# Performance work log

Hardware: AMD Instinct MI355X
Metric: run time of the kernel (lower is better)

Reference implementation:

```python
import jax, jax.numpy as jnp
import numpy as np

BLOCK_SIZE = 256
N_EMBED = 384
HEAD_SIZE = 64


def setup_inputs() -> dict:
    key = jax.random.key(0)
    kx, kq, kk, kv = jax.random.split(key, 4)
    B, T = 256, 256
    x = jax.random.normal(kx, (B, T, N_EMBED), dtype=jnp.float32)
    # nn.Linear(n_embed, head_size, bias=False): y = x @ W.T with W [head, embed].
    # We store the transposed weight [embed, head] so forward is x @ W.
    scale = 1.0 / np.sqrt(N_EMBED)
    Wq = jax.random.normal(kq, (N_EMBED, HEAD_SIZE), dtype=jnp.float32) * scale
    Wk = jax.random.normal(kk, (N_EMBED, HEAD_SIZE), dtype=jnp.float32) * scale
    Wv = jax.random.normal(kv, (N_EMBED, HEAD_SIZE), dtype=jnp.float32) * scale
    return {"x": x, "Wq": Wq, "Wk": Wk, "Wv": Wv}


def reference(x, Wq, Wk, Wv):
    B, T, C = x.shape  # C == N_EMBED
    q = jnp.einsum('btc,ch->bth', x, Wq)
    k = jnp.einsum('btc,ch->bth', x, Wk)
    v = jnp.einsum('btc,ch->bth', x, Wv)
    # NOTE: original scales by 1/sqrt(C) where C = embed dim (384), not head_size.
    wei = jnp.einsum('bth,bsh->bts', q, k) / jnp.sqrt(jnp.float32(C))
    causal = jnp.tril(jnp.ones((T, T), dtype=bool))
    wei = jnp.where(causal, wei, -jnp.inf)
    wei = jax.nn.softmax(wei, axis=-1)
    # dropout is identity in eval mode (reference is deterministic)
    out = jnp.einsum('bts,bsh->bth', wei, v)
    return out
```

## Files before the change

### kernel.cpp

```cpp
#include <hip/hip_runtime.h>


typedef short s16x8 __attribute__((ext_vector_type(8)));
typedef float f32x4 __attribute__((ext_vector_type(4)));
typedef float f32x2 __attribute__((ext_vector_type(2)));
typedef unsigned u32x4 __attribute__((ext_vector_type(4)));
typedef __bf16 bf16x2t __attribute__((ext_vector_type(2)));

#define MFMA16(a, b, c) __builtin_amdgcn_mfma_f32_16x16x32_bf16((a), (b), (c), 0, 0, 0)

__device__ __forceinline__ unsigned short f2bf(float f) {
  return __builtin_bit_cast(unsigned short, (__bf16)f);
}
__device__ __forceinline__ unsigned cvt2(float a, float b) {
  f32x2 t; t[0] = a; t[1] = b;
  bf16x2t r = __builtin_convertvector(t, bf16x2t);
  return __builtin_bit_cast(unsigned, r);
}
__device__ __forceinline__ s16x8 cvt8(float4 a, float4 b) {
  u32x4 u;
  u[0] = cvt2(a.x, a.y); u[1] = cvt2(a.z, a.w);
  u[2] = cvt2(b.x, b.y); u[3] = cvt2(b.z, b.w);
  return __builtin_bit_cast(s16x8, u);
}

__global__ __launch_bounds__(256) void wcvt(
    const float* __restrict__ Wq, const float* __restrict__ Wk,
    const float* __restrict__ Wv, unsigned short* __restrict__ Wt_sw) {
  int idx = blockIdx.x * 256 + threadIdx.x;
  int j = idx & 7;
  int c = idx >> 3;
  int n15 = c & 15;
  int q4 = (c >> 4) & 3;
  int g = c >> 6;
  int nt = g % 12;
  int kc = g / 12;
  int n = nt * 16 + n15;
  int kk = kc * 32 + q4 * 8 + j;
  const float* src = (n < 64) ? Wq : (n < 128) ? Wk : Wv;
  float v = src[kk * 64 + (n & 63)];
  if (n < 64) v *= 0.05103103630798287f;
  Wt_sw[idx] = f2bf(v);
}

__global__ __launch_bounds__(512) void fused_attn(
    const float* __restrict__ x, const unsigned short* __restrict__ Wt_sw,
    float* __restrict__ out) {
  __shared__ __align__(16) unsigned short q_l[16384];
  __shared__ __align__(16) unsigned short k_l[16384];
  __shared__ __align__(16) unsigned short v_l[16384];
  __shared__ __align__(16) unsigned short w_l[6144];
  const int b = blockIdx.x;
  const int tid = threadIdx.x;
  const int wv = tid >> 6;
  const int lane = tid & 63;
  const int n15 = lane & 15;
  const int q4 = lane >> 4;

  {
    const int rb0 = wv * 32;
    f32x4 acc[12][2];
#pragma unroll
    for (int i = 0; i < 12; ++i)
#pragma unroll
      for (int t = 0; t < 2; ++t) acc[i][t] = (f32x4){0.f, 0.f, 0.f, 0.f};

    const float* xp0 = x + ((long)b * 256 + rb0 + n15) * 384 + q4 * 8;
    const float* xp1 = xp0 + 16 * 384;
    float4 c00 = *reinterpret_cast<const float4*>(xp0);
    float4 c01 = *reinterpret_cast<const float4*>(xp0 + 4);
    float4 c10 = *reinterpret_cast<const float4*>(xp1);
    float4 c11 = *reinterpret_cast<const float4*>(xp1 + 4);

    const uint4* Wv4 = reinterpret_cast<const uint4*>(Wt_sw);
    uint4* wl4 = reinterpret_cast<uint4*>(w_l);
    uint4 wpa = Wv4[tid];
    uint4 wpb;
    if (tid < 256) wpb = Wv4[512 + tid];

    for (int kc = 0; kc < 12; ++kc) {
      __syncthreads();
      wl4[tid] = wpa;
      if (tid < 256) wl4[512 + tid] = wpb;
      __syncthreads();

      const int nkc = (kc < 11) ? kc + 1 : 11;
      wpa = Wv4[nkc * 768 + tid];
      if (tid < 256) wpb = Wv4[nkc * 768 + 512 + tid];
      float4 p00 = *reinterpret_cast<const float4*>(xp0 + nkc * 32);
      float4 p01 = *reinterpret_cast<const float4*>(xp0 + nkc * 32 + 4);
      float4 p10 = *reinterpret_cast<const float4*>(xp1 + nkc * 32);
      float4 p11 = *reinterpret_cast<const float4*>(xp1 + nkc * 32 + 4);

      s16x8 xa[2];
      xa[0] = cvt8(c00, c01);
      xa[1] = cvt8(c10, c11);

#pragma unroll
      for (int nt = 0; nt < 12; ++nt) {
        s16x8 wf = *reinterpret_cast<const s16x8*>(&w_l[nt * 512 + lane * 8]);
        if (nt < 8) {
          acc[nt][0] = MFMA16(wf, xa[0], acc[nt][0]);
          acc[nt][1] = MFMA16(wf, xa[1], acc[nt][1]);
        } else {
          acc[nt][0] = MFMA16(xa[0], wf, acc[nt][0]);
          acc[nt][1] = MFMA16(xa[1], wf, acc[nt][1]);
        }
      }
      c00 = p00; c01 = p01; c10 = p10; c11 = p11;
    }

#pragma unroll
    for (int t = 0; t < 2; ++t) {
      const int rb = rb0 + t * 16;
      const int qtile = rb >> 4;
#pragma unroll
      for (int mt = 0; mt < 4; ++mt) {
        const int off = ((qtile * 2 + (mt >> 1)) * 64 + (2 * (mt & 1) + (q4 >> 1)) * 16 + n15) * 8
                        + (q4 & 1) * 4;
        uint2 sq, sk;
        sq.x = cvt2(acc[mt][t][0], acc[mt][t][1]);
        sq.y = cvt2(acc[mt][t][2], acc[mt][t][3]);
        sk.x = cvt2(acc[4 + mt][t][0], acc[4 + mt][t][1]);
        sk.y = cvt2(acc[4 + mt][t][2], acc[4 + mt][t][3]);
        *reinterpret_cast<uint2*>(&q_l[off]) = sq;
        *reinterpret_cast<uint2*>(&k_l[off]) = sk;
      }
      const int s0 = rb + q4 * 4;
#pragma unroll
      for (int nt = 0; nt < 4; ++nt) {
        const int off = (((s0 >> 5) * 4 + nt) * 64 + ((s0 >> 3) & 3) * 16 + n15) * 8 + (s0 & 7);
        uint2 sv;
        sv.x = cvt2(acc[8 + nt][t][0], acc[8 + nt][t][1]);
        sv.y = cvt2(acc[8 + nt][t][2], acc[8 + nt][t][3]);
        *reinterpret_cast<uint2*>(&v_l[off]) = sv;
      }
    }
  }
  __syncthreads();

  const int laneA = ((q4 & 1) << 5) + n15;
  const bool hi = (q4 >> 1) != 0;
#pragma unroll
  for (int half = 0; half < 2; ++half) {
    const int qt = half ? (15 - wv) : wv;

    const s16x8 qf0 = *reinterpret_cast<const s16x8*>(&q_l[(qt * 2 + 0) * 512 + lane * 8]);
    const s16x8 qf1 = *reinterpret_cast<const s16x8*>(&q_l[(qt * 2 + 1) * 512 + lane * 8]);

    uint2 pk[16];
    float psum = 0.f;
    s16x8 kf0 = *reinterpret_cast<const s16x8*>(&k_l[0 * 512 + lane * 8]);
    s16x8 kf1 = *reinterpret_cast<const s16x8*>(&k_l[1 * 512 + lane * 8]);
#pragma unroll 16
    for (int ct = 0; ct < 16; ++ct) {
      if (ct > qt) break;
      const int nc = (ct < qt) ? ct + 1 : ct;
      s16x8 nf0 = *reinterpret_cast<const s16x8*>(&k_l[(nc * 2 + 0) * 512 + lane * 8]);
      s16x8 nf1 = *reinterpret_cast<const s16x8*>(&k_l[(nc * 2 + 1) * 512 + lane * 8]);
      f32x4 a = (f32x4){0.f, 0.f, 0.f, 0.f};
      a = MFMA16(kf0, qf0, a);
      a = MFMA16(kf1, qf1, a);
      const bool diag = (ct == qt);
      float p[4];
#pragma unroll
      for (int e = 0; e < 4; ++e) {
        p[e] = (diag && (q4 * 4 + e > n15)) ? 0.f : __expf(a[e]);
        psum += p[e];
      }
      pk[ct].x = cvt2(p[0], p[1]);
      pk[ct].y = cvt2(p[2], p[3]);
      kf0 = nf0; kf1 = nf1;
    }
    psum += __shfl_xor(psum, 16);
    psum += __shfl_xor(psum, 32);
    const float rn_col = 1.0f / psum;

    f32x4 O[4];
#pragma unroll
    for (int nt = 0; nt < 4; ++nt) O[nt] = (f32x4){0.f, 0.f, 0.f, 0.f};
    const int nk = (qt + 2) >> 1;
    s16x8 vf[4], vn[4];
#pragma unroll
    for (int nt = 0; nt < 4; ++nt)
      vf[nt] = *reinterpret_cast<const s16x8*>(&v_l[nt * 512 + lane * 8]);
#pragma unroll 8
    for (int kc = 0; kc < 8; ++kc) {
      if (kc >= nk) break;
      const int ncc = (kc + 1 < nk) ? kc + 1 : kc;
#pragma unroll
      for (int nt = 0; nt < 4; ++nt)
        vn[nt] = *reinterpret_cast<const s16x8*>(&v_l[(ncc * 4 + nt) * 512 + lane * 8]);
      const uint2 t0 = pk[2 * kc];
      const uint2 t1 = (2 * kc + 1 <= qt) ? pk[2 * kc + 1] : make_uint2(0u, 0u);
      unsigned r0a = __shfl(t0.x, laneA),      r0b = __shfl(t0.y, laneA);
      unsigned r0c = __shfl(t0.x, laneA + 16), r0d = __shfl(t0.y, laneA + 16);
      unsigned r1a = __shfl(t1.x, laneA),      r1b = __shfl(t1.y, laneA);
      unsigned r1c = __shfl(t1.x, laneA + 16), r1d = __shfl(t1.y, laneA + 16);
      u32x4 u;
      u[0] = hi ? r1a : r0a; u[1] = hi ? r1b : r0b;
      u[2] = hi ? r1c : r0c; u[3] = hi ? r1d : r0d;
      s16x8 pf = __builtin_bit_cast(s16x8, u);
#pragma unroll
      for (int nt = 0; nt < 4; ++nt) {
        O[nt] = MFMA16(pf, vf[nt], O[nt]);
        vf[nt] = vn[nt];
      }
    }
    float rnm[4];
#pragma unroll
    for (int e = 0; e < 4; ++e) rnm[e] = __shfl(rn_col, q4 * 4 + e);
#pragma unroll
    for (int nt = 0; nt < 4; ++nt)
#pragma unroll
      for (int e = 0; e < 4; ++e)
        out[(size_t)(b * 256 + qt * 16 + q4 * 4 + e) * 64 + nt * 16 + n15] = O[nt][e] * rnm[e];
  }
}

extern "C" void kernel_launch(void* const* d_in, const int* in_sizes, int n_in,
                              void* d_out, int out_size, void* d_ws, size_t ws_size,
                              hipStream_t stream) {
  const float* x  = (const float*)d_in[0];
  const float* Wq = (const float*)d_in[1];
  const float* Wk = (const float*)d_in[2];
  const float* Wv = (const float*)d_in[3];
  float* out = (float*)d_out;

  unsigned short* Wt_sw = (unsigned short*)d_ws;

  wcvt<<<288, 256, 0, stream>>>(Wq, Wk, Wv, Wt_sw);
  fused_attn<<<256, 512, 0, stream>>>(x, Wt_sw, out);
}
```

Before: 173.6 us.

## Use 1024-thread blocks with one query tile per wave and register-resident Q

The block grows from 8 to 16 waves, so each wave projects 16 rows instead of 32 and handles a single causal query tile instead of two balanced halves. Q fragments stay in registers through shuffles, which removes the q_l shared buffer. The weight tile is double-buffered in LDS, cutting one barrier per k-step. The QK^T/exp and PV phases are fused into one loop, so the 16-entry P register array goes away. The trade-off is that per-wave causal work becomes unbalanced (wave 15 does 16 tiles, wave 0 does 1), and the larger block may force fewer registers per thread.

New measurement: 167.4 us. -3.6%, faster.

```diff
diff --git a/kernel.cpp b/kernel.cpp
--- a/kernel.cpp
+++ b/kernel.cpp
@@ -21,6 +21,16 @@
   u32x4 u;
   u[0] = cvt2(a.x, a.y); u[1] = cvt2(a.z, a.w);
   u[2] = cvt2(b.x, b.y); u[3] = cvt2(b.z, b.w);
+  return __builtin_bit_cast(s16x8, u);
+}
+__device__ __forceinline__ s16x8 asm_frag(uint2 t0, uint2 t1, int laneA, bool hi) {
+  unsigned r0a = __shfl(t0.x, laneA),      r0b = __shfl(t0.y, laneA);
+  unsigned r0c = __shfl(t0.x, laneA + 16), r0d = __shfl(t0.y, laneA + 16);
+  unsigned r1a = __shfl(t1.x, laneA),      r1b = __shfl(t1.y, laneA);
+  unsigned r1c = __shfl(t1.x, laneA + 16), r1d = __shfl(t1.y, laneA + 16);
+  u32x4 u;
+  u[0] = hi ? r1a : r0a; u[1] = hi ? r1b : r0b;
+  u[2] = hi ? r1c : r0c; u[3] = hi ? r1d : r0d;
   return __builtin_bit_cast(s16x8, u);
 }
 
@@ -43,13 +53,12 @@
   Wt_sw[idx] = f2bf(v);
 }
 
-__global__ __launch_bounds__(512) void fused_attn(
+__global__ __launch_bounds__(1024, 4) void fused_attn(
     const float* __restrict__ x, const unsigned short* __restrict__ Wt_sw,
     float* __restrict__ out) {
-  __shared__ __align__(16) unsigned short q_l[16384];
   __shared__ __align__(16) unsigned short k_l[16384];
   __shared__ __align__(16) unsigned short v_l[16384];
-  __shared__ __align__(16) unsigned short w_l[6144];
+  __shared__ __align__(16) unsigned short w_l[12288];
   const int b = blockIdx.x;
   const int tid = threadIdx.x;
   const int wv = tid >> 6;
@@ -57,165 +66,135 @@
   const int n15 = lane & 15;
   const int q4 = lane >> 4;
 
-  {
-    const int rb0 = wv * 32;
-    f32x4 acc[12][2];
-#pragma unroll
-    for (int i = 0; i < 12; ++i)
-#pragma unroll
-      for (int t = 0; t < 2; ++t) acc[i][t] = (f32x4){0.f, 0.f, 0.f, 0.f};
-
-    const float* xp0 = x + ((long)b * 256 + rb0 + n15) * 384 + q4 * 8;
-    const float* xp1 = xp0 + 16 * 384;
-    float4 c00 = *reinterpret_cast<const float4*>(xp0);
-    float4 c01 = *reinterpret_cast<const float4*>(xp0 + 4);
-    float4 c10 = *reinterpret_cast<const float4*>(xp1);
-    float4 c11 = *reinterpret_cast<const float4*>(xp1 + 4);
-
-    const uint4* Wv4 = reinterpret_cast<const uint4*>(Wt_sw);
-    uint4* wl4 = reinterpret_cast<uint4*>(w_l);
-    uint4 wpa = Wv4[tid];
-    uint4 wpb;
-    if (tid < 256) wpb = Wv4[512 + tid];
-
-    for (int kc = 0; kc < 12; ++kc) {
-      __syncthreads();
-      wl4[tid] = wpa;
-      if (tid < 256) wl4[512 + tid] = wpb;
-      __syncthreads();
-
-      const int nkc = (kc < 11) ? kc + 1 : 11;
-      wpa = Wv4[nkc * 768 + tid];
-      if (tid < 256) wpb = Wv4[nkc * 768 + 512 + tid];
-      float4 p00 = *reinterpret_cast<const float4*>(xp0 + nkc * 32);
-      float4 p01 = *reinterpret_cast<const float4*>(xp0 + nkc * 32 + 4);
-      float4 p10 = *reinterpret_cast<const float4*>(xp1 + nkc * 32);
-      float4 p11 = *reinterpret_cast<const float4*>(xp1 + nkc * 32 + 4);
-
-      s16x8 xa[2];
-      xa[0] = cvt8(c00, c01);
-      xa[1] = cvt8(c10, c11);
-
-#pragma unroll
-      for (int nt = 0; nt < 12; ++nt) {
-        s16x8 wf = *reinterpret_cast<const s16x8*>(&w_l[nt * 512 + lane * 8]);
-        if (nt < 8) {
-          acc[nt][0] = MFMA16(wf, xa[0], acc[nt][0]);
-          acc[nt][1] = MFMA16(wf, xa[1], acc[nt][1]);
-        } else {
-          acc[nt][0] = MFMA16(xa[0], wf, acc[nt][0]);
-          acc[nt][1] = MFMA16(xa[1], wf, acc[nt][1]);
-        }
-      }
-      c00 = p00; c01 = p01; c10 = p10; c11 = p11;
-    }
-
-#pragma unroll
-    for (int t = 0; t < 2; ++t) {
-      const int rb = rb0 + t * 16;
-      const int qtile = rb >> 4;
-#pragma unroll
-      for (int mt = 0; mt < 4; ++mt) {
-        const int off = ((qtile * 2 + (mt >> 1)) * 64 + (2 * (mt & 1) + (q4 >> 1)) * 16 + n15) * 8
-                        + (q4 & 1) * 4;
-        uint2 sq, sk;
-        sq.x = cvt2(acc[mt][t][0], acc[mt][t][1]);
-        sq.y = cvt2(acc[mt][t][2], acc[mt][t][3]);
-        sk.x = cvt2(acc[4 + mt][t][0], acc[4 + mt][t][1]);
-        sk.y = cvt2(acc[4 + mt][t][2], acc[4 + mt][t][3]);
-        *reinterpret_cast<uint2*>(&q_l[off]) = sq;
-        *reinterpret_cast<uint2*>(&k_l[off]) = sk;
-      }
-      const int s0 = rb + q4 * 4;
-#pragma unroll
-      for (int nt = 0; nt < 4; ++nt) {
-        const int off = (((s0 >> 5) * 4 + nt) * 64 + ((s0 >> 3) & 3) * 16 + n15) * 8 + (s0 & 7);
-        uint2 sv;
-        sv.x = cvt2(acc[8 + nt][t][0], acc[8 + nt][t][1]);
-        sv.y = cvt2(acc[8 + nt][t][2], acc[8 + nt][t][3]);
-        *reinterpret_cast<uint2*>(&v_l[off]) = sv;
-      }
-    }
-  }
-  __syncthreads();
+  f32x4 acc[12];
+#pragma unroll
+  for (int i = 0; i < 12; ++i) acc[i] = (f32x4){0.f, 0.f, 0.f, 0.f};
+
+  const float* xp = x + ((long)b * 256 + wv * 16 + n15) * 384 + q4 * 8;
+  float4 f0a = *reinterpret_cast<const float4*>(xp);
+  float4 f0b = *reinterpret_cast<const float4*>(xp + 4);
+  float4 f1a = *reinterpret_cast<const float4*>(xp + 32);
+  float4 f1b = *reinterpret_cast<const float4*>(xp + 36);
+
+  const uint4* Wv4 = reinterpret_cast<const uint4*>(Wt_sw);
+  uint4* wl4 = reinterpret_cast<uint4*>(w_l);
+  uint4 wreg;
+  if (tid < 768) wreg = Wv4[tid];
+
+  for (int kc = 0; kc < 12; ++kc) {
+    if (tid < 768) wl4[(kc & 1) * 768 + tid] = wreg;
+    __syncthreads();
+    if (kc < 11 && tid < 768) wreg = Wv4[(kc + 1) * 768 + tid];
+    const int nkc = (kc < 10) ? kc + 2 : 11;
+    float4 pa = *reinterpret_cast<const float4*>(xp + nkc * 32);
+    float4 pb = *reinterpret_cast<const float4*>(xp + nkc * 32 + 4);
+
+    s16x8 xa = cvt8(f0a, f0b);
+    const unsigned short* wbuf = w_l + (kc & 1) * 6144;
+#pragma unroll
+    for (int nt = 0; nt < 12; ++nt) {
+      s16x8 wf = *reinterpret_cast<const s16x8*>(&wbuf[nt * 512 + lane * 8]);
+      if (nt < 8) acc[nt] = MFMA16(wf, xa, acc[nt]);
+      else        acc[nt] = MFMA16(xa, wf, acc[nt]);
+    }
+    f0a = f1a; f0b = f1b; f1a = pa; f1b = pb;
+  }
+
+  uint2 pkq[4];
+#pragma unroll
+  for (int mt = 0; mt < 4; ++mt) {
+    pkq[mt].x = cvt2(acc[mt][0], acc[mt][1]);
+    pkq[mt].y = cvt2(acc[mt][2], acc[mt][3]);
+  }
+#pragma unroll
+  for (int mt = 0; mt < 4; ++mt) {
+    const int off = ((wv * 2 + (mt >> 1)) * 64 + (2 * (mt & 1) + (q4 >> 1)) * 16 + n15) * 8
+                    + (q4 & 1) * 4;
+    uint2 sk;
+    sk.x = cvt2(acc[4 + mt][0], acc[4 + mt][1]);
+    sk.y = cvt2(acc[4 + mt][2], acc[4 + mt][3]);
+    *reinterpret_cast<uint2*>(&k_l[off]) = sk;
+  }
+  const int s0 = wv * 16 + q4 * 4;
+#pragma unroll
+  for (int nt = 0; nt < 4; ++nt) {
+    const int off = (((s0 >> 5) * 4 + nt) * 64 + ((s0 >> 3) & 3) * 16 + n15) * 8 + (s0 & 7);
+    uint2 sv;
+    sv.x = cvt2(acc[8 + nt][0], acc[8 + nt][1]);
+    sv.y = cvt2(acc[8 + nt][2], acc[8 + nt][3]);
+    *reinterpret_cast<uint2*>(&v_l[off]) = sv;
+  }
 
   const int laneA = ((q4 & 1) << 5) + n15;
   const bool hi = (q4 >> 1) != 0;
-#pragma unroll
-  for (int half = 0; half < 2; ++half) {
-    const int qt = half ? (15 - wv) : wv;
-
-    const s16x8 qf0 = *reinterpret_cast<const s16x8*>(&q_l[(qt * 2 + 0) * 512 + lane * 8]);
-    const s16x8 qf1 = *reinterpret_cast<const s16x8*>(&q_l[(qt * 2 + 1) * 512 + lane * 8]);
-
-    uint2 pk[16];
-    float psum = 0.f;
-    s16x8 kf0 = *reinterpret_cast<const s16x8*>(&k_l[0 * 512 + lane * 8]);
-    s16x8 kf1 = *reinterpret_cast<const s16x8*>(&k_l[1 * 512 + lane * 8]);
-#pragma unroll 16
-    for (int ct = 0; ct < 16; ++ct) {
-      if (ct > qt) break;
-      const int nc = (ct < qt) ? ct + 1 : ct;
-      s16x8 nf0 = *reinterpret_cast<const s16x8*>(&k_l[(nc * 2 + 0) * 512 + lane * 8]);
-      s16x8 nf1 = *reinterpret_cast<const s16x8*>(&k_l[(nc * 2 + 1) * 512 + lane * 8]);
-      f32x4 a = (f32x4){0.f, 0.f, 0.f, 0.f};
-      a = MFMA16(kf0, qf0, a);
-      a = MFMA16(kf1, qf1, a);
-      const bool diag = (ct == qt);
+  const s16x8 qf0 = asm_frag(pkq[0], pkq[1], laneA, hi);
+  const s16x8 qf1 = asm_frag(pkq[2], pkq[3], laneA, hi);
+  __syncthreads();
+
+  const int qt = wv;
+  const f32x4 zf = (f32x4){0.f, 0.f, 0.f, 0.f};
+  f32x4 O[4];
+#pragma unroll
+  for (int nt = 0; nt < 4; ++nt) O[nt] = zf;
+  float psum = 0.f;
+  const int nk = (qt + 2) >> 1;
+#pragma unroll 8
+  for (int kc = 0; kc < 8; ++kc) {
+    if (kc >= nk) break;
+    const int ct0 = 2 * kc;
+    const bool has1 = (ct0 + 1 <= qt);
+    s16x8 kf0 = *reinterpret_cast<const s16x8*>(&k_l[(ct0 * 2 + 0) * 512 + lane * 8]);
+    s16x8 kf1 = *reinterpret_cast<const s16x8*>(&k_l[(ct0 * 2 + 1) * 512 + lane * 8]);
+    f32x4 a0 = MFMA16(kf0, qf0, zf);
+    f32x4 a1 = MFMA16(kf1, qf1, zf);
+    uint2 t0, t1;
+    {
+      f32x4 s = a0 + a1;
+      const bool diag = (ct0 == qt);
       float p[4];
 #pragma unroll
       for (int e = 0; e < 4; ++e) {
-        p[e] = (diag && (q4 * 4 + e > n15)) ? 0.f : __expf(a[e]);
+        p[e] = (diag && (q4 * 4 + e > n15)) ? 0.f : __expf(s[e]);
         psum += p[e];
       }
-      pk[ct].x = cvt2(p[0], p[1]);
-      pk[ct].y = cvt2(p[2], p[3]);
-      kf0 = nf0; kf1 = nf1;
-    }
-    psum += __shfl_xor(psum, 16);
-    psum += __shfl_xor(psum, 32);
-    const float rn_col = 1.0f / psum;
-
-    f32x4 O[4];
-#pragma unroll
-    for (int nt = 0; nt < 4; ++nt) O[nt] = (f32x4){0.f, 0.f, 0.f, 0.f};
-    const int nk = (qt + 2) >> 1;
-    s16x8 vf[4], vn[4];
-#pragma unroll
-    for (int nt = 0; nt < 4; ++nt)
-      vf[nt] = *reinterpret_cast<const s16x8*>(&v_l[nt * 512 + lane * 8]);
-#pragma unroll 8
-    for (int kc = 0; kc < 8; ++kc) {
-      if (kc >= nk) break;
-      const int ncc = (kc + 1 < nk) ? kc + 1 : kc;
-#pragma unroll
-      for (int nt = 0; nt < 4; ++nt)
-        vn[nt] = *reinterpret_cast<const s16x8*>(&v_l[(ncc * 4 + nt) * 512 + lane * 8]);
-      const uint2 t0 = pk[2 * kc];
-      const uint2 t1 = (2 * kc + 1 <= qt) ? pk[2 * kc + 1] : make_uint2(0u, 0u);
-      unsigned r0a = __shfl(t0.x, laneA),      r0b = __shfl(t0.y, laneA);
-      unsigned r0c = __shfl(t0.x, laneA + 16), r0d = __shfl(t0.y, laneA + 16);
-      unsigned r1a = __shfl(t1.x, laneA),      r1b = __shfl(t1.y, laneA);
-      unsigned r1c = __shfl(t1.x, laneA + 16), r1d = __shfl(t1.y, laneA + 16);
-      u32x4 u;
-      u[0] = hi ? r1a : r0a; u[1] = hi ? r1b : r0b;
-      u[2] = hi ? r1c : r0c; u[3] = hi ? r1d : r0d;
-      s16x8 pf = __builtin_bit_cast(s16x8, u);
-#pragma unroll
-      for (int nt = 0; nt < 4; ++nt) {
-        O[nt] = MFMA16(pf, vf[nt], O[nt]);
-        vf[nt] = vn[nt];
+      t0.x = cvt2(p[0], p[1]); t0.y = cvt2(p[2], p[3]);
+    }
+    if (has1) {
+      const int ct1 = ct0 + 1;
+      s16x8 kg0 = *reinterpret_cast<const s16x8*>(&k_l[(ct1 * 2 + 0) * 512 + lane * 8]);
+      s16x8 kg1 = *reinterpret_cast<const s16x8*>(&k_l[(ct1 * 2 + 1) * 512 + lane * 8]);
+      f32x4 b0 = MFMA16(kg0, qf0, zf);
+      f32x4 b1 = MFMA16(kg1, qf1, zf);
+      f32x4 s = b0 + b1;
+      const bool diag = (ct1 == qt);
+      float p[4];
+#pragma unroll
+      for (int e = 0; e < 4; ++e) {
+        p[e] = (diag && (q4 * 4 + e > n15)) ? 0.f : __expf(s[e]);
+        psum += p[e];
       }
-    }
-    float rnm[4];
-#pragma unroll
-    for (int e = 0; e < 4; ++e) rnm[e] = __shfl(rn_col, q4 * 4 + e);
-#pragma unroll
-    for (int nt = 0; nt < 4; ++nt)
-#pragma unroll
-      for (int e = 0; e < 4; ++e)
-        out[(size_t)(b * 256 + qt * 16 + q4 * 4 + e) * 64 + nt * 16 + n15] = O[nt][e] * rnm[e];
-  }
+      t1.x = cvt2(p[0], p[1]); t1.y = cvt2(p[2], p[3]);
+    } else {
+      t1 = make_uint2(0u, 0u);
+    }
+    s16x8 pf = asm_frag(t0, t1, laneA, hi);
+#pragma unroll
+    for (int nt = 0; nt < 4; ++nt) {
+      s16x8 vf = *reinterpret_cast<const s16x8*>(&v_l[(kc * 4 + nt) * 512 + lane * 8]);
+      O[nt] = MFMA16(pf, vf, O[nt]);
+    }
+  }
+  psum += __shfl_xor(psum, 16);
+  psum += __shfl_xor(psum, 32);
+  const float rn_col = 1.0f / psum;
+  float rnm[4];
+#pragma unroll
+  for (int e = 0; e < 4; ++e) rnm[e] = __shfl(rn_col, q4 * 4 + e);
+#pragma unroll
+  for (int nt = 0; nt < 4; ++nt)
+#pragma unroll
+    for (int e = 0; e < 4; ++e)
+      out[(size_t)(b * 256 + qt * 16 + q4 * 4 + e) * 64 + nt * 16 + n15] = O[nt][e] * rnm[e];
 }
 
 extern "C" void kernel_launch(void* const* d_in, const int* in_sizes, int n_in,
@@ -230,5 +209,5 @@
   unsigned short* Wt_sw = (unsigned short*)d_ws;
 
   wcvt<<<288, 256, 0, stream>>>(Wq, Wk, Wv, Wt_sw);
-  fused_attn<<<256, 512, 0, stream>>>(x, Wt_sw, out);
-}
+  fused_attn<<<256, 1024, 0, stream>>>(x, Wt_sw, out);
+}
```
